# Optimization experiments

Measured on AMD Instinct MI355X. Metric: run time of the kernel, lower is better.

The kernel has to match this reference:

```python
import jax, jax.numpy as jnp
import numpy as np

EPS = 1e-6
LN_EPS = 1e-6


def _bd(x, W):
    # Block-diagonal dense: x (B, F) viewed as (B, H, D); W (H, D, D)
    B = x.shape[0]
    H, D, _ = W.shape
    return jnp.einsum('bhd,hde->bhe', x.reshape(B, H, D), W).reshape(B, H * D)


def setup_inputs() -> dict:
    key = jax.random.key(0)
    B, F, H, D, K = 4096, 1024, 4, 256, 4
    ks = jax.random.split(key, 24)
    inp = {}
    inp['inputs'] = jax.random.normal(ks[0], (B, F), jnp.float32)
    inp['c'] = jax.random.normal(ks[1], (B, F), jnp.float32)
    inp['n'] = jax.random.uniform(ks[2], (B, F), jnp.float32)  # nonzero -> general stabilizer branch
    inp['m'] = jax.random.normal(ks[3], (B, F), jnp.float32)
    inp['h'] = jax.random.normal(ks[4], (B, F), jnp.float32)
    inp['conv_state'] = jax.random.normal(ks[5], (B, K, F), jnp.float32)
    inp['conv_kernel'] = jax.random.normal(ks[6], (K, F), jnp.float32) * 0.1
    inp['conv_bias'] = jax.random.normal(ks[7], (F,), jnp.float32) * 0.1
    for idx, name in enumerate(['Wi', 'Wf', 'Wz', 'Wo', 'Ri', 'Rf', 'Rz', 'Ro']):
        inp[name] = jax.random.normal(ks[8 + idx], (H, D, D), jnp.float32) * 0.02
    for idx, name in enumerate(['bi', 'bf', 'bz', 'bo']):
        inp[name] = jax.random.normal(ks[16 + idx], (F,), jnp.float32) * 0.1
    inp['ln_scale'] = jnp.ones((H, D), jnp.float32)
    return inp


def reference(inputs, c, n, m, h, conv_state, conv_kernel, conv_bias,
              Wi, Wf, Wz, Wo, Ri, Rf, Rz, Ro, bi, bf, bz, bo, ln_scale):
    B = inputs.shape[0]
    H, D = ln_scale.shape

    # Causal depthwise conv, single step: shift state, append new input
    new_conv_state = jnp.concatenate([conv_state[:, 1:, :], inputs[:, None, :]], axis=1)  # (B,K,F)
    conv_x = jnp.einsum('bkf,kf->bf', new_conv_state, conv_kernel) + conv_bias
    conv_act = jax.nn.silu(conv_x)

    # Gate pre-activations: input (block-diag) + recurrent (block-diag) + bias
    i = _bd(conv_act, Wi) + _bd(h, Ri) + bi
    f = _bd(conv_act, Wf) + _bd(h, Rf) + bf
    z = _bd(inputs, Wz) + _bd(h, Rz) + bz
    o = _bd(inputs, Wo) + _bd(h, Ro) + bo

    o_gate = jax.nn.sigmoid(o)
    log_f = -jax.nn.softplus(-f)  # forget_activation == 'sigmoid'

    # Stabilizer
    m_new = jnp.where(jnp.all(n == 0.0), i, jnp.maximum(log_f + m, i))
    i_p = jnp.minimum(jnp.exp(i - m_new), 1.0)
    f_p = jnp.minimum(jnp.exp(log_f + m - m_new), 1.0)

    c_new = f_p * c + i_p * jnp.tanh(z)
    n_new = f_p * n + i_p
    h_new = o_gate * (c_new / jnp.maximum(n_new, EPS))

    # Multi-head LayerNorm over head_dim (scale only, no bias)
    y = h_new.reshape(B, H, D)
    mu = jnp.mean(y, axis=-1, keepdims=True)
    var = jnp.var(y, axis=-1, keepdims=True)
    out = ((y - mu) * jax.lax.rsqrt(var + LN_EPS) * ln_scale).reshape(B, H * D)

    return (out, c_new, n_new, m_new, h_new, new_conv_state)
```

## Files before the change

kernel.cpp:

```cpp
#include <hip/hip_runtime.h>

#define B_N 4096
#define F_N 1024
#define H_N 4
#define D_N 256
#define BF_ELEMS (B_N * F_N)

typedef unsigned short u16;
typedef __bf16 bf16x8 __attribute__((ext_vector_type(8)));
typedef float f32x4 __attribute__((ext_vector_type(4)));
typedef u16 u16x4 __attribute__((ext_vector_type(4)));
typedef u16 u16x8 __attribute__((ext_vector_type(8)));

__device__ __forceinline__ u16 f2bf(float v) {
    union { float f; unsigned u; } x; x.f = v;
    unsigned r = x.u + 0x7fffu + ((x.u >> 16) & 1u);
    return (u16)(r >> 16);
}

__device__ __forceinline__ float bf2f(u16 v) {
    union { unsigned u; float f; } x; x.u = ((unsigned)v) << 16;
    return x.f;
}

__global__ __launch_bounds__(256) void kprep(
    const float* __restrict__ inputs, const float* __restrict__ cs,
    const float* __restrict__ ck, const float* __restrict__ cb,
    const float* __restrict__ h, const float* __restrict__ n,
    const float* W0, const float* W1, const float* W2, const float* W3,
    const float* W4, const float* W5, const float* W6, const float* W7,
    float* __restrict__ ncs_out, u16* __restrict__ convact,
    u16* __restrict__ hbf, u16* __restrict__ inbf,
    u16* __restrict__ wt, int* __restrict__ flag) {
    __shared__ float tile[32][33];
    int bid = blockIdx.x;
    int t = threadIdx.x;
    if (bid < 4096) {
        int idx = bid * 256 + t;
        int flat = idx << 2;
        int b = flat >> 10;
        int f = flat & 1023;
        const f32x4 x  = *(const f32x4*)(inputs + flat);
        const f32x4 c1 = *(const f32x4*)(cs + b * 4096 + 1024 + f);
        const f32x4 c2 = *(const f32x4*)(cs + b * 4096 + 2048 + f);
        const f32x4 c3 = *(const f32x4*)(cs + b * 4096 + 3072 + f);
        const f32x4 k0 = *(const f32x4*)(ck + f);
        const f32x4 k1 = *(const f32x4*)(ck + 1024 + f);
        const f32x4 k2 = *(const f32x4*)(ck + 2048 + f);
        const f32x4 k3 = *(const f32x4*)(ck + 3072 + f);
        const f32x4 bias = *(const f32x4*)(cb + f);
        const f32x4 h4 = *(const f32x4*)(h + flat);
        const f32x4 nv = *(const f32x4*)(n + flat);

        bool any = (nv[0] != 0.f) || (nv[1] != 0.f) || (nv[2] != 0.f) || (nv[3] != 0.f);
        unsigned long long msk = __ballot(any);
        if (msk && (t & 63) == 0) *flag = 1;

        u16x4 ca, hb, ib;
        #pragma unroll
        for (int q = 0; q < 4; ++q) {
            float v = c1[q] * k0[q] + c2[q] * k1[q] + c3[q] * k2[q] + x[q] * k3[q] + bias[q];
            float a = v / (1.f + expf(-v));
            ca[q] = f2bf(a);
            hb[q] = f2bf(h4[q]);
            ib[q] = f2bf(x[q]);
        }
        *(u16x4*)(convact + flat) = ca;
        *(u16x4*)(hbf + flat) = hb;
        *(u16x4*)(inbf + flat) = ib;

        float* ob = ncs_out + b * 4096 + f;
        *(f32x4*)(ob)        = c1;
        *(f32x4*)(ob + 1024) = c2;
        *(f32x4*)(ob + 2048) = c3;
        *(f32x4*)(ob + 3072) = x;
    } else {
        int wb = bid - 4096;
        int gx = wb & 63;
        int hd = (wb >> 6) & 3;
        int mat = wb >> 8;
        const float* tab[8] = {W0, W1, W2, W3, W4, W5, W6, W7};
        const float* src = tab[mat] + hd * 65536;
        u16* dst = wt + (mat * 4 + hd) * 65536;
        int tx = t & 31, ty = t >> 5;
        int bx = (gx & 7) * 32;
        int by = (gx >> 3) * 32;
        #pragma unroll
        for (int r = 0; r < 4; ++r)
            tile[ty + r * 8][tx] = src[(by + ty + r * 8) * 256 + bx + tx];
        __syncthreads();
        #pragma unroll
        for (int r = 0; r < 4; ++r)
            dst[(by >> 5) * 8192 + (bx + ty + r * 8) * 32 + tx] = f2bf(tile[tx][ty + r * 8]);
    }
}

__global__ __launch_bounds__(1024, 4) void kfused(
    const u16* __restrict__ convact, const u16* __restrict__ inbf,
    const u16* __restrict__ hbf, const u16* __restrict__ wt2,
    const float* __restrict__ bgi, const float* __restrict__ bgf,
    const float* __restrict__ bgz, const float* __restrict__ bgo,
    const float* __restrict__ c, const float* __restrict__ n,
    const float* __restrict__ m, const float* __restrict__ ln_scale,
    const int* __restrict__ flagp, float* __restrict__ out) {
    __shared__ __align__(16) u16 smem[32768];

    int t = threadIdx.x;
    int mtile = blockIdx.x;
    int hd = blockIdx.y;
    int row0 = mtile * 32;

    {
        int r = t >> 5, gd = t & 31;
        int gl = gd ^ (r & 7);
        size_t soff = (size_t)(row0 + r) * 1024 + hd * 256 + gl * 8;
        __builtin_amdgcn_global_load_lds(
            (const __attribute__((address_space(1))) void*)(convact + soff),
            (__attribute__((address_space(3))) void*)(&smem[t * 8]), 16, 0, 0);
        __builtin_amdgcn_global_load_lds(
            (const __attribute__((address_space(1))) void*)(inbf + soff),
            (__attribute__((address_space(3))) void*)(&smem[8192 + t * 8]), 16, 0, 0);
        __builtin_amdgcn_global_load_lds(
            (const __attribute__((address_space(1))) void*)(hbf + soff),
            (__attribute__((address_space(3))) void*)(&smem[16384 + t * 8]), 16, 0, 0);
    }
    __syncthreads();

    int lane = t & 63, lr = lane & 15, lk = lane >> 4;
    int w = t >> 6;
    int g = w >> 2;
    int q = w & 3;

    f32x4 acc[2][4];
    #pragma unroll
    for (int i = 0; i < 2; ++i)
        #pragma unroll
        for (int j = 0; j < 4; ++j)
            acc[i][j] = (f32x4){0.f, 0.f, 0.f, 0.f};

    const u16* bW = wt2 + (size_t)(g * 4 + hd) * 65536;
    const u16* bR = wt2 + (size_t)((g + 4) * 4 + hd) * 65536;
    int bcol = (q * 64 + lr) * 32 + lk * 8;
    int aselW = (g < 2) ? 0 : 8192;
    int grs = (lr & 7);

    #pragma unroll 4
    for (int ks = 0; ks < 8; ++ks) {
        bf16x8 b0 = *(const bf16x8*)(bW + ks * 8192 + bcol);
        bf16x8 b1 = *(const bf16x8*)(bW + ks * 8192 + bcol + 512);
        bf16x8 b2 = *(const bf16x8*)(bW + ks * 8192 + bcol + 1024);
        bf16x8 b3 = *(const bf16x8*)(bW + ks * 8192 + bcol + 1536);
        int gr = (ks * 4 + lk) ^ grs;
        bf16x8 a0 = *(const bf16x8*)&smem[aselW + lr * 256 + gr * 8];
        bf16x8 a1 = *(const bf16x8*)&smem[aselW + (16 + lr) * 256 + gr * 8];
        acc[0][0] = __builtin_amdgcn_mfma_f32_16x16x32_bf16(a0, b0, acc[0][0], 0, 0, 0);
        acc[0][1] = __builtin_amdgcn_mfma_f32_16x16x32_bf16(a0, b1, acc[0][1], 0, 0, 0);
        acc[0][2] = __builtin_amdgcn_mfma_f32_16x16x32_bf16(a0, b2, acc[0][2], 0, 0, 0);
        acc[0][3] = __builtin_amdgcn_mfma_f32_16x16x32_bf16(a0, b3, acc[0][3], 0, 0, 0);
        acc[1][0] = __builtin_amdgcn_mfma_f32_16x16x32_bf16(a1, b0, acc[1][0], 0, 0, 0);
        acc[1][1] = __builtin_amdgcn_mfma_f32_16x16x32_bf16(a1, b1, acc[1][1], 0, 0, 0);
        acc[1][2] = __builtin_amdgcn_mfma_f32_16x16x32_bf16(a1, b2, acc[1][2], 0, 0, 0);
        acc[1][3] = __builtin_amdgcn_mfma_f32_16x16x32_bf16(a1, b3, acc[1][3], 0, 0, 0);
    }
    #pragma unroll 4
    for (int ks = 0; ks < 8; ++ks) {
        bf16x8 b0 = *(const bf16x8*)(bR + ks * 8192 + bcol);
        bf16x8 b1 = *(const bf16x8*)(bR + ks * 8192 + bcol + 512);
        bf16x8 b2 = *(const bf16x8*)(bR + ks * 8192 + bcol + 1024);
        bf16x8 b3 = *(const bf16x8*)(bR + ks * 8192 + bcol + 1536);
        int gr = (ks * 4 + lk) ^ grs;
        bf16x8 a0 = *(const bf16x8*)&smem[16384 + lr * 256 + gr * 8];
        bf16x8 a1 = *(const bf16x8*)&smem[16384 + (16 + lr) * 256 + gr * 8];
        acc[0][0] = __builtin_amdgcn_mfma_f32_16x16x32_bf16(a0, b0, acc[0][0], 0, 0, 0);
        acc[0][1] = __builtin_amdgcn_mfma_f32_16x16x32_bf16(a0, b1, acc[0][1], 0, 0, 0);
        acc[0][2] = __builtin_amdgcn_mfma_f32_16x16x32_bf16(a0, b2, acc[0][2], 0, 0, 0);
        acc[0][3] = __builtin_amdgcn_mfma_f32_16x16x32_bf16(a0, b3, acc[0][3], 0, 0, 0);
        acc[1][0] = __builtin_amdgcn_mfma_f32_16x16x32_bf16(a1, b0, acc[1][0], 0, 0, 0);
        acc[1][1] = __builtin_amdgcn_mfma_f32_16x16x32_bf16(a1, b1, acc[1][1], 0, 0, 0);
        acc[1][2] = __builtin_amdgcn_mfma_f32_16x16x32_bf16(a1, b2, acc[1][2], 0, 0, 0);
        acc[1][3] = __builtin_amdgcn_mfma_f32_16x16x32_bf16(a1, b3, acc[1][3], 0, 0, 0);
    }

    __syncthreads();
    {
        const float* bt = (g == 0 ? bgi : g == 1 ? bgf : g == 2 ? bgz : bgo)
                          + hd * 256 + q * 64;
        #pragma unroll
        for (int nt = 0; nt < 4; ++nt) {
            float bv = bt[nt * 16 + lr];
            int col = g * 256 + q * 64 + nt * 16 + lr;
            #pragma unroll
            for (int mt = 0; mt < 2; ++mt)
                #pragma unroll
                for (int r = 0; r < 4; ++r)
                    smem[(mt * 16 + lk * 4 + r) * 1024 + col] = f2bf(acc[mt][nt][r] + bv);
        }
    }
    __syncthreads();

    {
        int prow = t >> 5;
        int e0 = (t & 31) * 8;
        u16x8 iv = *(const u16x8*)&smem[prow * 1024 + e0];
        u16x8 fv = *(const u16x8*)&smem[prow * 1024 + 256 + e0];
        u16x8 zv = *(const u16x8*)&smem[prow * 1024 + 512 + e0];
        u16x8 ov = *(const u16x8*)&smem[prow * 1024 + 768 + e0];
        size_t idx = (size_t)(row0 + prow) * 1024 + hd * 256 + e0;
        f32x4 cv0 = *(const f32x4*)(c + idx), cv1 = *(const f32x4*)(c + idx + 4);
        f32x4 nv0 = *(const f32x4*)(n + idx), nv1 = *(const f32x4*)(n + idx + 4);
        f32x4 mv0 = *(const f32x4*)(m + idx), mv1 = *(const f32x4*)(m + idx + 4);
        f32x4 sc0 = *(const f32x4*)(ln_scale + hd * 256 + e0);
        f32x4 sc1 = *(const f32x4*)(ln_scale + hd * 256 + e0 + 4);
        int flag = *flagp;

        float cn[8], nn[8], mn[8], hn[8];
        float s = 0.f, ss = 0.f;
        #pragma unroll
        for (int e = 0; e < 8; ++e) {
            float I = bf2f(iv[e]);
            float Fg = bf2f(fv[e]);
            float Z = bf2f(zv[e]);
            float O = bf2f(ov[e]);
            float cvq = (e < 4) ? cv0[e] : cv1[e - 4];
            float nvq = (e < 4) ? nv0[e] : nv1[e - 4];
            float mvq = (e < 4) ? mv0[e] : mv1[e - 4];
            float og = 1.f / (1.f + expf(-O));
            float lf = (Fg >= 0.f) ? -log1pf(expf(-Fg)) : (Fg - log1pf(expf(Fg)));
            float mnew = flag ? fmaxf(lf + mvq, I) : I;
            float ip = fminf(expf(I - mnew), 1.f);
            float fp = fminf(expf(lf + mvq - mnew), 1.f);
            float cnew = fp * cvq + ip * tanhf(Z);
            float nnew = fp * nvq + ip;
            float hnew = og * (cnew / fmaxf(nnew, 1e-6f));
            cn[e] = cnew; nn[e] = nnew; mn[e] = mnew; hn[e] = hnew;
            s += hnew; ss += hnew * hnew;
        }
        #pragma unroll
        for (int off = 16; off >= 1; off >>= 1) {
            s  += __shfl_xor(s, off);
            ss += __shfl_xor(ss, off);
        }
        float mu = s * (1.f / 256.f);
        float var = ss * (1.f / 256.f) - mu * mu;
        float rs = rsqrtf(var + 1e-6f);

        f32x4 o0, o1, c0, c1, n0, n1, m0, m1, h0, h1;
        #pragma unroll
        for (int e = 0; e < 4; ++e) {
            o0[e] = (hn[e] - mu) * rs * sc0[e];
            o1[e] = (hn[e + 4] - mu) * rs * sc1[e];
            c0[e] = cn[e]; c1[e] = cn[e + 4];
            n0[e] = nn[e]; n1[e] = nn[e + 4];
            m0[e] = mn[e]; m1[e] = mn[e + 4];
            h0[e] = hn[e]; h1[e] = hn[e + 4];
        }
        *(f32x4*)(out + idx) = o0;
        *(f32x4*)(out + idx + 4) = o1;
        *(f32x4*)(out + (size_t)BF_ELEMS + idx) = c0;
        *(f32x4*)(out + (size_t)BF_ELEMS + idx + 4) = c1;
        *(f32x4*)(out + 2 * (size_t)BF_ELEMS + idx) = n0;
        *(f32x4*)(out + 2 * (size_t)BF_ELEMS + idx + 4) = n1;
        *(f32x4*)(out + 3 * (size_t)BF_ELEMS + idx) = m0;
        *(f32x4*)(out + 3 * (size_t)BF_ELEMS + idx + 4) = m1;
        *(f32x4*)(out + 4 * (size_t)BF_ELEMS + idx) = h0;
        *(f32x4*)(out + 4 * (size_t)BF_ELEMS + idx + 4) = h1;
    }
}

extern "C" void kernel_launch(void* const* d_in, const int* in_sizes, int n_in,
                              void* d_out, int out_size, void* d_ws, size_t ws_size,
                              hipStream_t stream) {
    const float* inputs = (const float*)d_in[0];
    const float* c = (const float*)d_in[1];
    const float* n = (const float*)d_in[2];
    const float* m = (const float*)d_in[3];
    const float* h = (const float*)d_in[4];
    const float* conv_state = (const float*)d_in[5];
    const float* conv_kernel = (const float*)d_in[6];
    const float* conv_bias = (const float*)d_in[7];
    const float* W[8];
    for (int i = 0; i < 8; ++i) W[i] = (const float*)d_in[8 + i];
    const float* bgi = (const float*)d_in[16];
    const float* bgf = (const float*)d_in[17];
    const float* bgz = (const float*)d_in[18];
    const float* bgo = (const float*)d_in[19];
    const float* ln_scale = (const float*)d_in[20];
    float* out = (float*)d_out;

    char* ws = (char*)d_ws;
    int* flag = (int*)ws;
    u16* convact = (u16*)(ws + 256);
    u16* hbf = convact + BF_ELEMS;
    u16* inbf = hbf + BF_ELEMS;
    u16* wt2 = inbf + BF_ELEMS;

    hipMemsetAsync(flag, 0, 4, stream);
    kprep<<<6144, 256, 0, stream>>>(inputs, conv_state, conv_kernel, conv_bias, h, n,
                                    W[0], W[1], W[2], W[3], W[4], W[5], W[6], W[7],
                                    out + 5 * (size_t)BF_ELEMS, convact, hbf, inbf, wt2, flag);
    kfused<<<dim3(128, 4), 1024, 0, stream>>>(convact, inbf, hbf, wt2,
                                              bgi, bgf, bgz, bgo,
                                              c, n, m, ln_scale, flag, out);
}
```

Baseline: 128.8 us.

## Double-buffer weight and activation K-slices in LDS with 64-row tiles

The fused gate GEMM kernel now stages both B (weight) and A (activation) K-slices into LDS through async global_load_lds, double-buffered so the next slice loads while the current one is multiplied. Previously each wave read weights straight from global memory. The M tile per block doubles to 64 rows, halving the grid to 256 blocks and doubling per-wave accumulators (4x4 MFMA tiles), which raises weight reuse. The cost is 144KB of LDS per block, more registers, a sync on every K step, and fewer blocks than CUs, which may hurt occupancy and load balance.

```diff
diff --git a/kernel.cpp b/kernel.cpp
--- a/kernel.cpp
+++ b/kernel.cpp
@@ -95,176 +95,193 @@
     }
 }
 
-__global__ __launch_bounds__(1024, 4) void kfused(
+__global__ __launch_bounds__(1024) void kfused(
     const u16* __restrict__ convact, const u16* __restrict__ inbf,
     const u16* __restrict__ hbf, const u16* __restrict__ wt2,
     const float* __restrict__ bgi, const float* __restrict__ bgf,
     const float* __restrict__ bgz, const float* __restrict__ bgo,
-    const float* __restrict__ c, const float* __restrict__ n,
-    const float* __restrict__ m, const float* __restrict__ ln_scale,
+    const float* __restrict__ cin, const float* __restrict__ nin,
+    const float* __restrict__ min, const float* __restrict__ ln_scale,
     const int* __restrict__ flagp, float* __restrict__ out) {
-    __shared__ __align__(16) u16 smem[32768];
+    __shared__ __align__(16) u16 smem[73728];
 
     int t = threadIdx.x;
     int mtile = blockIdx.x;
     int hd = blockIdx.y;
-    int row0 = mtile * 32;
-
-    {
-        int r = t >> 5, gd = t & 31;
-        int gl = gd ^ (r & 7);
-        size_t soff = (size_t)(row0 + r) * 1024 + hd * 256 + gl * 8;
-        __builtin_amdgcn_global_load_lds(
-            (const __attribute__((address_space(1))) void*)(convact + soff),
-            (__attribute__((address_space(3))) void*)(&smem[t * 8]), 16, 0, 0);
-        __builtin_amdgcn_global_load_lds(
-            (const __attribute__((address_space(1))) void*)(inbf + soff),
-            (__attribute__((address_space(3))) void*)(&smem[8192 + t * 8]), 16, 0, 0);
-        __builtin_amdgcn_global_load_lds(
-            (const __attribute__((address_space(1))) void*)(hbf + soff),
-            (__attribute__((address_space(3))) void*)(&smem[16384 + t * 8]), 16, 0, 0);
-    }
-    __syncthreads();
+    int row0 = mtile * 64;
+
+    int srow = t >> 2;
+    int sgl = (t & 3) ^ (srow & 3);
+
+    #define GLDS(src, dstoff)                                                     \
+        __builtin_amdgcn_global_load_lds(                                         \
+            (const __attribute__((address_space(1))) void*)(src),                 \
+            (__attribute__((address_space(3))) void*)(&smem[dstoff]), 16, 0, 0)
+
+    #define STAGE_B(dbase, matoff, ks) do {                                       \
+        _Pragma("unroll")                                                         \
+        for (int rd = 0; rd < 4; ++rd)                                            \
+            GLDS(wt2 + (size_t)(((matoff) + rd) * 4 + hd) * 65536 + (ks) * 8192   \
+                     + srow * 32 + sgl * 8,                                       \
+                 (dbase) + 4096 + rd * 8192 + t * 8);                             \
+    } while (0)
+
+    #define STAGE_A0(dbase, ks) do {                                              \
+        if (t < 512) {                                                            \
+            const u16* asrc = (t < 256) ? convact : inbf;                         \
+            int tt = t & 255;                                                     \
+            int rr = tt >> 2;                                                     \
+            int gg = (tt & 3) ^ (rr & 3);                                         \
+            GLDS(asrc + (size_t)(row0 + rr) * 1024 + hd * 256 + (ks) * 32 + gg * 8, \
+                 (dbase) + (t < 256 ? 0 : 2048) + tt * 8);                        \
+        }                                                                         \
+    } while (0)
+
+    #define STAGE_A1(dbase, ks) do {                                              \
+        if (t < 256) {                                                            \
+            int rr = t >> 2;                                                      \
+            int gg = (t & 3) ^ (rr & 3);                                          \
+            GLDS(hbf + (size_t)(row0 + rr) * 1024 + hd * 256 + (ks) * 32 + gg * 8, \
+                 (dbase) + t * 8);                                                \
+        }                                                                         \
+    } while (0)
 
     int lane = t & 63, lr = lane & 15, lk = lane >> 4;
     int w = t >> 6;
     int g = w >> 2;
     int q = w & 3;
-
-    f32x4 acc[2][4];
+    int gl = lk ^ (lr & 3);
+
+    f32x4 acc[4][4];
     #pragma unroll
-    for (int i = 0; i < 2; ++i)
+    for (int i = 0; i < 4; ++i)
         #pragma unroll
         for (int j = 0; j < 4; ++j)
             acc[i][j] = (f32x4){0.f, 0.f, 0.f, 0.f};
 
-    const u16* bW = wt2 + (size_t)(g * 4 + hd) * 65536;
-    const u16* bR = wt2 + (size_t)((g + 4) * 4 + hd) * 65536;
-    int bcol = (q * 64 + lr) * 32 + lk * 8;
-    int aselW = (g < 2) ? 0 : 8192;
-    int grs = (lr & 7);
-
-    #pragma unroll 4
-    for (int ks = 0; ks < 8; ++ks) {
-        bf16x8 b0 = *(const bf16x8*)(bW + ks * 8192 + bcol);
-        bf16x8 b1 = *(const bf16x8*)(bW + ks * 8192 + bcol + 512);
-        bf16x8 b2 = *(const bf16x8*)(bW + ks * 8192 + bcol + 1024);
-        bf16x8 b3 = *(const bf16x8*)(bW + ks * 8192 + bcol + 1536);
-        int gr = (ks * 4 + lk) ^ grs;
-        bf16x8 a0 = *(const bf16x8*)&smem[aselW + lr * 256 + gr * 8];
-        bf16x8 a1 = *(const bf16x8*)&smem[aselW + (16 + lr) * 256 + gr * 8];
-        acc[0][0] = __builtin_amdgcn_mfma_f32_16x16x32_bf16(a0, b0, acc[0][0], 0, 0, 0);
-        acc[0][1] = __builtin_amdgcn_mfma_f32_16x16x32_bf16(a0, b1, acc[0][1], 0, 0, 0);
-        acc[0][2] = __builtin_amdgcn_mfma_f32_16x16x32_bf16(a0, b2, acc[0][2], 0, 0, 0);
-        acc[0][3] = __builtin_amdgcn_mfma_f32_16x16x32_bf16(a0, b3, acc[0][3], 0, 0, 0);
-        acc[1][0] = __builtin_amdgcn_mfma_f32_16x16x32_bf16(a1, b0, acc[1][0], 0, 0, 0);
-        acc[1][1] = __builtin_amdgcn_mfma_f32_16x16x32_bf16(a1, b1, acc[1][1], 0, 0, 0);
-        acc[1][2] = __builtin_amdgcn_mfma_f32_16x16x32_bf16(a1, b2, acc[1][2], 0, 0, 0);
-        acc[1][3] = __builtin_amdgcn_mfma_f32_16x16x32_bf16(a1, b3, acc[1][3], 0, 0, 0);
-    }
-    #pragma unroll 4
-    for (int ks = 0; ks < 8; ++ks) {
-        bf16x8 b0 = *(const bf16x8*)(bR + ks * 8192 + bcol);
-        bf16x8 b1 = *(const bf16x8*)(bR + ks * 8192 + bcol + 512);
-        bf16x8 b2 = *(const bf16x8*)(bR + ks * 8192 + bcol + 1024);
-        bf16x8 b3 = *(const bf16x8*)(bR + ks * 8192 + bcol + 1536);
-        int gr = (ks * 4 + lk) ^ grs;
-        bf16x8 a0 = *(const bf16x8*)&smem[16384 + lr * 256 + gr * 8];
-        bf16x8 a1 = *(const bf16x8*)&smem[16384 + (16 + lr) * 256 + gr * 8];
-        acc[0][0] = __builtin_amdgcn_mfma_f32_16x16x32_bf16(a0, b0, acc[0][0], 0, 0, 0);
-        acc[0][1] = __builtin_amdgcn_mfma_f32_16x16x32_bf16(a0, b1, acc[0][1], 0, 0, 0);
-        acc[0][2] = __builtin_amdgcn_mfma_f32_16x16x32_bf16(a0, b2, acc[0][2], 0, 0, 0);
-        acc[0][3] = __builtin_amdgcn_mfma_f32_16x16x32_bf16(a0, b3, acc[0][3], 0, 0, 0);
-        acc[1][0] = __builtin_amdgcn_mfma_f32_16x16x32_bf16(a1, b0, acc[1][0], 0, 0, 0);
-        acc[1][1] = __builtin_amdgcn_mfma_f32_16x16x32_bf16(a1, b1, acc[1][1], 0, 0, 0);
-        acc[1][2] = __builtin_amdgcn_mfma_f32_16x16x32_bf16(a1, b2, acc[1][2], 0, 0, 0);
-        acc[1][3] = __builtin_amdgcn_mfma_f32_16x16x32_bf16(a1, b3, acc[1][3], 0, 0, 0);
-    }
-
+    #define COMPUTE(dbase, abase) do {                                            \
+        bf16x8 a[4], bb[4];                                                       \
+        _Pragma("unroll")                                                         \
+        for (int mi = 0; mi < 4; ++mi)                                            \
+            a[mi] = *(const bf16x8*)&smem[(abase) + (mi * 16 + lr) * 32 + gl * 8]; \
+        _Pragma("unroll")                                                         \
+        for (int ni = 0; ni < 4; ++ni)                                            \
+            bb[ni] = *(const bf16x8*)&smem[(dbase) + 4096 + g * 8192              \
+                                           + (q * 64 + ni * 16 + lr) * 32 + gl * 8]; \
+        _Pragma("unroll")                                                         \
+        for (int mi = 0; mi < 4; ++mi)                                            \
+            _Pragma("unroll")                                                     \
+            for (int ni = 0; ni < 4; ++ni)                                        \
+                acc[mi][ni] = __builtin_amdgcn_mfma_f32_16x16x32_bf16(            \
+                    a[mi], bb[ni], acc[mi][ni], 0, 0, 0);                         \
+    } while (0)
+
+    STAGE_B(0, 0, 0);
+    STAGE_A0(0, 0);
     __syncthreads();
+
+    #pragma unroll 2
+    for (int kt = 0; kt < 8; ++kt) {
+        int cb = (kt & 1) ? 36864 : 0;
+        int nb = (kt & 1) ? 0 : 36864;
+        if (kt < 7) { STAGE_B(nb, 0, kt + 1); STAGE_A0(nb, kt + 1); }
+        else        { STAGE_B(nb, 4, 0);      STAGE_A1(nb, 0); }
+        int abase = cb + (g < 2 ? 0 : 2048);
+        COMPUTE(cb, abase);
+        __syncthreads();
+    }
+    #pragma unroll 2
+    for (int kt = 0; kt < 8; ++kt) {
+        int cb = (kt & 1) ? 36864 : 0;
+        int nb = (kt & 1) ? 0 : 36864;
+        if (kt < 7) { STAGE_B(nb, 4, kt + 1); STAGE_A1(nb, kt + 1); }
+        COMPUTE(cb, cb);
+        __syncthreads();
+    }
+
     {
         const float* bt = (g == 0 ? bgi : g == 1 ? bgf : g == 2 ? bgz : bgo)
                           + hd * 256 + q * 64;
         #pragma unroll
-        for (int nt = 0; nt < 4; ++nt) {
-            float bv = bt[nt * 16 + lr];
-            int col = g * 256 + q * 64 + nt * 16 + lr;
+        for (int ni = 0; ni < 4; ++ni) {
+            float bv = bt[ni * 16 + lr];
+            int col = g * 256 + q * 64 + ni * 16 + lr;
             #pragma unroll
-            for (int mt = 0; mt < 2; ++mt)
+            for (int mi = 0; mi < 4; ++mi)
                 #pragma unroll
                 for (int r = 0; r < 4; ++r)
-                    smem[(mt * 16 + lk * 4 + r) * 1024 + col] = f2bf(acc[mt][nt][r] + bv);
+                    smem[(mi * 16 + lk * 4 + r) * 1024 + col] = f2bf(acc[mi][ni][r] + bv);
         }
     }
     __syncthreads();
 
     {
-        int prow = t >> 5;
-        int e0 = (t & 31) * 8;
-        u16x8 iv = *(const u16x8*)&smem[prow * 1024 + e0];
-        u16x8 fv = *(const u16x8*)&smem[prow * 1024 + 256 + e0];
-        u16x8 zv = *(const u16x8*)&smem[prow * 1024 + 512 + e0];
-        u16x8 ov = *(const u16x8*)&smem[prow * 1024 + 768 + e0];
-        size_t idx = (size_t)(row0 + prow) * 1024 + hd * 256 + e0;
-        f32x4 cv0 = *(const f32x4*)(c + idx), cv1 = *(const f32x4*)(c + idx + 4);
-        f32x4 nv0 = *(const f32x4*)(n + idx), nv1 = *(const f32x4*)(n + idx + 4);
-        f32x4 mv0 = *(const f32x4*)(m + idx), mv1 = *(const f32x4*)(m + idx + 4);
-        f32x4 sc0 = *(const f32x4*)(ln_scale + hd * 256 + e0);
-        f32x4 sc1 = *(const f32x4*)(ln_scale + hd * 256 + e0 + 4);
+        int prow = t >> 4;
+        int c0 = (t & 15) * 16;
+        size_t idx = (size_t)(row0 + prow) * 1024 + hd * 256 + c0;
         int flag = *flagp;
 
-        float cn[8], nn[8], mn[8], hn[8];
+        float cn[16], nn[16], mn[16], hn[16];
         float s = 0.f, ss = 0.f;
         #pragma unroll
-        for (int e = 0; e < 8; ++e) {
-            float I = bf2f(iv[e]);
-            float Fg = bf2f(fv[e]);
-            float Z = bf2f(zv[e]);
-            float O = bf2f(ov[e]);
-            float cvq = (e < 4) ? cv0[e] : cv1[e - 4];
-            float nvq = (e < 4) ? nv0[e] : nv1[e - 4];
-            float mvq = (e < 4) ? mv0[e] : mv1[e - 4];
-            float og = 1.f / (1.f + expf(-O));
-            float lf = (Fg >= 0.f) ? -log1pf(expf(-Fg)) : (Fg - log1pf(expf(Fg)));
-            float mnew = flag ? fmaxf(lf + mvq, I) : I;
-            float ip = fminf(expf(I - mnew), 1.f);
-            float fp = fminf(expf(lf + mvq - mnew), 1.f);
-            float cnew = fp * cvq + ip * tanhf(Z);
-            float nnew = fp * nvq + ip;
-            float hnew = og * (cnew / fmaxf(nnew, 1e-6f));
-            cn[e] = cnew; nn[e] = nnew; mn[e] = mnew; hn[e] = hnew;
-            s += hnew; ss += hnew * hnew;
-        }
-        #pragma unroll
-        for (int off = 16; off >= 1; off >>= 1) {
-            s  += __shfl_xor(s, off);
-            ss += __shfl_xor(ss, off);
+        for (int e8 = 0; e8 < 2; ++e8) {
+            u16x8 iv = *(const u16x8*)&smem[prow * 1024 + c0 + e8 * 8];
+            u16x8 fv = *(const u16x8*)&smem[prow * 1024 + 256 + c0 + e8 * 8];
+            u16x8 zv = *(const u16x8*)&smem[prow * 1024 + 512 + c0 + e8 * 8];
+            u16x8 ov = *(const u16x8*)&smem[prow * 1024 + 768 + c0 + e8 * 8];
+            #pragma unroll
+            for (int j = 0; j < 8; ++j) {
+                int e = e8 * 8 + j;
+                float I = bf2f(iv[j]);
+                float Fg = bf2f(fv[j]);
+                float Z = bf2f(zv[j]);
+                float O = bf2f(ov[j]);
+                float cvq = cin[idx + e];
+                float nvq = nin[idx + e];
+                float mvq = min[idx + e];
+                float og = 1.f / (1.f + expf(-O));
+                float lf = (Fg >= 0.f) ? -log1pf(expf(-Fg)) : (Fg - log1pf(expf(Fg)));
+                float mnew = flag ? fmaxf(lf + mvq, I) : I;
+                float ip = fminf(expf(I - mnew), 1.f);
+                float fp = fminf(expf(lf + mvq - mnew), 1.f);
+                float cnew = fp * cvq + ip * tanhf(Z);
+                float nnew = fp * nvq + ip;
+                float hnew = og * (cnew / fmaxf(nnew, 1e-6f));
+                cn[e] = cnew; nn[e] = nnew; mn[e] = mnew; hn[e] = hnew;
+                s += hnew; ss += hnew * hnew;
+            }
+        }
+        #pragma unroll
+        for (int off = 8; off >= 1; off >>= 1) {
+            s  += __shfl_xor(s, off, 16);
+            ss += __shfl_xor(ss, off, 16);
         }
         float mu = s * (1.f / 256.f);
         float var = ss * (1.f / 256.f) - mu * mu;
         float rs = rsqrtf(var + 1e-6f);
 
-        f32x4 o0, o1, c0, c1, n0, n1, m0, m1, h0, h1;
-        #pragma unroll
-        for (int e = 0; e < 4; ++e) {
-            o0[e] = (hn[e] - mu) * rs * sc0[e];
-            o1[e] = (hn[e + 4] - mu) * rs * sc1[e];
-            c0[e] = cn[e]; c1[e] = cn[e + 4];
-            n0[e] = nn[e]; n1[e] = nn[e + 4];
-            m0[e] = mn[e]; m1[e] = mn[e + 4];
-            h0[e] = hn[e]; h1[e] = hn[e + 4];
-        }
-        *(f32x4*)(out + idx) = o0;
-        *(f32x4*)(out + idx + 4) = o1;
-        *(f32x4*)(out + (size_t)BF_ELEMS + idx) = c0;
-        *(f32x4*)(out + (size_t)BF_ELEMS + idx + 4) = c1;
-        *(f32x4*)(out + 2 * (size_t)BF_ELEMS + idx) = n0;
-        *(f32x4*)(out + 2 * (size_t)BF_ELEMS + idx + 4) = n1;
-        *(f32x4*)(out + 3 * (size_t)BF_ELEMS + idx) = m0;
-        *(f32x4*)(out + 3 * (size_t)BF_ELEMS + idx + 4) = m1;
-        *(f32x4*)(out + 4 * (size_t)BF_ELEMS + idx) = h0;
-        *(f32x4*)(out + 4 * (size_t)BF_ELEMS + idx + 4) = h1;
-    }
+        #pragma unroll
+        for (int v4 = 0; v4 < 4; ++v4) {
+            f32x4 o4, c4, n4, m4, h4;
+            #pragma unroll
+            for (int j = 0; j < 4; ++j) {
+                int e = v4 * 4 + j;
+                float sc = ln_scale[hd * 256 + c0 + e];
+                o4[j] = (hn[e] - mu) * rs * sc;
+                c4[j] = cn[e]; n4[j] = nn[e]; m4[j] = mn[e]; h4[j] = hn[e];
+            }
+            *(f32x4*)(out + idx + v4 * 4) = o4;
+            *(f32x4*)(out + (size_t)BF_ELEMS + idx + v4 * 4) = c4;
+            *(f32x4*)(out + 2 * (size_t)BF_ELEMS + idx + v4 * 4) = n4;
+            *(f32x4*)(out + 3 * (size_t)BF_ELEMS + idx + v4 * 4) = m4;
+            *(f32x4*)(out + 4 * (size_t)BF_ELEMS + idx + v4 * 4) = h4;
+        }
+    }
+    #undef COMPUTE
+    #undef STAGE_A1
+    #undef STAGE_A0
+    #undef STAGE_B
+    #undef GLDS
 }
 
 extern "C" void kernel_launch(void* const* d_in, const int* in_sizes, int n_in,
@@ -298,7 +315,7 @@
     kprep<<<6144, 256, 0, stream>>>(inputs, conv_state, conv_kernel, conv_bias, h, n,
                                     W[0], W[1], W[2], W[3], W[4], W[5], W[6], W[7],
                                     out + 5 * (size_t)BF_ELEMS, convact, hbf, inbf, wt2, flag);
-    kfused<<<dim3(128, 4), 1024, 0, stream>>>(convact, inbf, hbf, wt2,
-                                              bgi, bgf, bgz, bgo,
-                                              c, n, m, ln_scale, flag, out);
-}
+    kfused<<<dim3(64, 4), 1024, 0, stream>>>(convact, inbf, hbf, wt2,
+                                             bgi, bgf, bgz, bgo,
+                                             c, n, m, ln_scale, flag, out);
+}
```

Measured after the change: 137.8 us. 7.0% more time.
